# Performance work log

Hardware: AMD Instinct MI355X
Metric: run time of the kernel (lower is better)

The kernel has to match this reference:

```python
import jax, jax.numpy as jnp
import numpy as np
from jax import lax

K = 3          # kernel_size
G = 8          # group count in SIFA
EPS = 1e-5     # BN and GN eps


def _bn(x, g, b, m, v):
    # eval-mode BatchNorm2d over channel dim 1
    scale = (g / jnp.sqrt(v + EPS))[None, :, None, None]
    shift = (b - m * g / jnp.sqrt(v + EPS))[None, :, None, None]
    return x * scale + shift


def setup_inputs() -> dict:
    key = jax.random.key(0)
    ks = jax.random.split(key, 20)
    B, C, H, W, OUP = 8, 64, 128, 128, 128
    CE = C * K * K  # expanded channels = 576
    CG = C // G     # channels per group view = 8
    f32 = jnp.float32
    inp = {
        "x": jax.random.normal(ks[0], (B, C, H, W), f32),
        # depthwise generate conv: groups=C, out=C*K^2 -> OIHW [CE,1,K,K]
        "gen_w": jax.random.normal(ks[1], (CE, 1, K, K), f32) * 0.1,
        "gen_bn_g": jnp.ones((CE,), f32) + 0.1 * jax.random.normal(ks[2], (CE,), f32),
        "gen_bn_b": 0.1 * jax.random.normal(ks[3], (CE,), f32),
        "gen_bn_m": 0.05 * jax.random.normal(ks[4], (CE,), f32),
        "gen_bn_v": jax.random.uniform(ks[5], (CE,), f32, 0.5, 1.5),
        # GroupNorm(num_groups=CG, num_channels=CG) affine params
        "gn_w": jnp.ones((CG,), f32) + 0.1 * jax.random.normal(ks[6], (CG,), f32),
        "gn_b": 0.1 * jax.random.normal(ks[7], (CG,), f32),
        # gating params, shape (1, CG, 1, 1)
        "cweight": 0.1 * jax.random.normal(ks[8], (1, CG, 1, 1), f32),
        "cbias": jnp.ones((1, CG, 1, 1), f32) + 0.1 * jax.random.normal(ks[9], (1, CG, 1, 1), f32),
        "sweight": 0.1 * jax.random.normal(ks[10], (1, CG, 1, 1), f32),
        "sbias": jnp.ones((1, CG, 1, 1), f32) + 0.1 * jax.random.normal(ks[11], (1, CG, 1, 1), f32),
        "weights_add": jnp.asarray(0.5, f32),
        # final Conv: C -> OUP, k=K, s=K, p=0, bias=False + BN + SiLU
        "conv_w": jax.random.normal(ks[12], (OUP, C, K, K), f32) * (1.0 / np.sqrt(C * K * K)),
        "conv_bn_g": jnp.ones((OUP,), f32) + 0.1 * jax.random.normal(ks[13], (OUP,), f32),
        "conv_bn_b": 0.1 * jax.random.normal(ks[14], (OUP,), f32),
        "conv_bn_m": 0.05 * jax.random.normal(ks[15], (OUP,), f32),
        "conv_bn_v": jax.random.uniform(ks[16], (OUP,), f32, 0.5, 1.5),
    }
    return inp


def reference(x, gen_w, gen_bn_g, gen_bn_b, gen_bn_m, gen_bn_v,
              gn_w, gn_b, cweight, cbias, sweight, sbias, weights_add,
              conv_w, conv_bn_g, conv_bn_b, conv_bn_m, conv_bn_v):
    B, C, H, W = x.shape
    # --- generate: depthwise conv (groups=C) + BN + ReLU ---
    y = lax.conv_general_dilated(
        x, gen_w, window_strides=(1, 1), padding=[(K // 2, K // 2)] * 2,
        feature_group_count=C,
        dimension_numbers=("NCHW", "OIHW", "NCHW"))  # [B, C*K*K, H, W]
    y = jax.nn.relu(_bn(y, gen_bn_g, gen_bn_b, gen_bn_m, gen_bn_v))
    # --- rearrange 'b c (n1 n2) h w -> b c (h n1) (w n2)' ---
    y = y.reshape(B, C, K, K, H, W)          # (b, c, n1, n2, h, w)
    y = y.transpose(0, 1, 4, 2, 5, 3)        # (b, c, h, n1, w, n2)
    HK, WK = H * K, W * K
    y = y.reshape(B, C, HK, WK)
    # --- group view: (b*G, C//G, HK, WK) ---
    g = y.reshape(B * G, C // G, HK, WK)
    # channel gate: global avg pool -> affine -> sigmoid
    x_ch = jnp.mean(g, axis=(2, 3), keepdims=True)        # [B*G, CG, 1, 1]
    ch = g * jax.nn.sigmoid(cweight * x_ch + cbias)
    # spatial gate: per-channel GroupNorm (num_groups == num_channels)
    mu = jnp.mean(g, axis=(2, 3), keepdims=True)
    var = jnp.var(g, axis=(2, 3), keepdims=True)
    gnorm = (g - mu) / jnp.sqrt(var + EPS)
    gnorm = gnorm * gn_w[None, :, None, None] + gn_b[None, :, None, None]
    sp = g * jax.nn.sigmoid(sweight * gnorm + sbias)
    out = weights_add * ch + (1.0 - weights_add) * sp
    out = out.reshape(B, C, HK, WK)
    # --- final Conv: k=K, s=K, p=0, no bias + BN + SiLU ---
    z = lax.conv_general_dilated(
        out, conv_w, window_strides=(K, K), padding="VALID",
        dimension_numbers=("NCHW", "OIHW", "NCHW"))       # [B, OUP, H, W]
    z = _bn(z, conv_bn_g, conv_bn_b, conv_bn_m, conv_bn_v)
    return z * jax.nn.sigmoid(z)  # SiLU
```

## Files before the change

### kernel.cpp

```cpp
#include <hip/hip_runtime.h>
#include <math.h>


#define EPSF 1e-5f
typedef _Float16 v8h __attribute__((ext_vector_type(8)));
typedef float v4f __attribute__((ext_vector_type(4)));

static constexpr int C_ = 64, HW_ = 16384, W_ = 128;

static constexpr int WS_WFOLD = 0;
static constexpr int WS_SHIFT = 5184;
static constexpr int WS_BIAS  = 5760;
static constexpr int WS_GATE  = 5888;
static constexpr int WS_PART  = 7936;
static constexpr int WS_WH    = 12032;

__device__ __forceinline__ float sigmf(float v) { return 1.f / (1.f + __expf(-v)); }

__global__ __launch_bounds__(256) void k_fold(
    const float* __restrict__ gen_w,
    const float* __restrict__ gg, const float* __restrict__ gb,
    const float* __restrict__ gm, const float* __restrict__ gv,
    const float* __restrict__ conv_w,
    const float* __restrict__ cg, const float* __restrict__ cb,
    const float* __restrict__ cm, const float* __restrict__ cv,
    float* __restrict__ ws)
{
    int idx = blockIdx.x * 256 + threadIdx.x;
    _Float16* Whp = (_Float16*)(ws + WS_WH);
    if (idx < 131072) {
        int oup = idx >> 10, kk = idx & 1023, c = kk >> 4, j = kk & 15;
        float s = cg[oup] * rsqrtf(cv[oup] + EPSF);
        float v = (j < 9) ? conv_w[(oup * C_ + c) * 9 + j] * s : 0.f;
        Whp[idx] = (_Float16)v;
    } else if (idx < 136256) {
        int i = idx - 131072; int ce = i / 9;
        float s = gg[ce] * rsqrtf(gv[ce] + EPSF);
        ws[WS_WFOLD + i] = gen_w[i] * s;
    } else if (idx < 136832) {
        int ce = idx - 136256;
        float s = gg[ce] * rsqrtf(gv[ce] + EPSF);
        ws[WS_SHIFT + ce] = gb[ce] - gm[ce] * s;
    } else if (idx < 136960) {
        int oup = idx - 136832;
        float s = cg[oup] * rsqrtf(cv[oup] + EPSF);
        ws[WS_BIAS + oup] = cb[oup] - cm[oup] * s;
    }
}

__global__ __launch_bounds__(256) void k_stats(
    const float* __restrict__ x, const float* __restrict__ ws,
    float* __restrict__ part)
{
    __shared__ float xs[34 * 132];
    __shared__ float r1[256], r2[256];
    int bid = blockIdx.x; int b = bid >> 8; int c = (bid >> 2) & 63; int q = bid & 3;
    int t = threadIdx.x;
    const float* xp = x + (size_t)(b * C_ + c) * HW_;
    for (int i = t; i < 4420; i += 256) {
        int r = i / 130, cc = i - r * 130;
        int yy = q * 32 + r - 1, xx = cc - 1;
        float v = 0.f;
        if (yy >= 0 && yy < 128 && xx >= 0 && xx < 128) v = xp[yy * 128 + xx];
        xs[r * 132 + cc] = v;
    }
    __syncthreads();
    const float* wf = ws + WS_WFOLD + c * 81;
    const float* sh = ws + WS_SHIFT + c * 9;
    float s1 = 0.f, s2 = 0.f;
    for (int i = 0; i < 16; ++i) {
        int id = i * 256 + t; int row = id >> 7, col = id & 127;
        float nb[9];
#pragma unroll
        for (int dy = 0; dy < 3; ++dy)
#pragma unroll
            for (int dx = 0; dx < 3; ++dx) nb[dy * 3 + dx] = xs[(row + dy) * 132 + col + dx];
#pragma unroll
        for (int j = 0; j < 9; ++j) {
            float v = sh[j];
#pragma unroll
            for (int k = 0; k < 9; ++k) v = fmaf(wf[j * 9 + k], nb[k], v);
            v = fmaxf(v, 0.f);
            s1 += v; s2 = fmaf(v, v, s2);
        }
    }
    r1[t] = s1; r2[t] = s2;
    __syncthreads();
    for (int s = 128; s > 0; s >>= 1) {
        if (t < s) { r1[t] += r1[t + s]; r2[t] += r2[t + s]; }
        __syncthreads();
    }
    if (t == 0) { part[bid * 2] = r1[0]; part[bid * 2 + 1] = r2[0]; }
}

__global__ __launch_bounds__(256) void k_gate(
    const float* __restrict__ part,
    const float* __restrict__ cwt, const float* __restrict__ cbs,
    const float* __restrict__ swt, const float* __restrict__ sbs,
    const float* __restrict__ gnw, const float* __restrict__ gnb,
    const float* __restrict__ wadd, float4* __restrict__ gate)
{
    int i = blockIdx.x * 256 + threadIdx.x;
    if (i >= 512) return;
    int b = i >> 6, c = i & 63;
    float s1 = 0.f, s2 = 0.f;
    for (int q = 0; q < 4; ++q) {
        int pi = (b * 256 + c * 4 + q) * 2;
        s1 += part[pi]; s2 += part[pi + 1];
    }
    const float N = 9.f * 16384.f;
    float mean = s1 / N;
    float var = s2 / N - mean * mean;
    float inv = rsqrtf(var + EPSF);
    int cgi = c & 7;
    float wa = wadd[0];
    float cgt = sigmf(cwt[cgi] * mean + cbs[cgi]);
    float4 o;
    o.x = wa * cgt;
    o.y = 1.f - wa;
    o.z = swt[cgi] * gnw[cgi] * inv;
    o.w = swt[cgi] * (gnb[cgi] - mean * inv * gnw[cgi]) + sbs[cgi];
    gate[i] = o;
}

__global__ __launch_bounds__(256) void k_main(
    const float* __restrict__ x, const float* __restrict__ ws,
    float* __restrict__ out)
{
    __shared__ _Float16 W_s[128 * 64];
    __shared__ _Float16 u_s[128 * 64];
    __shared__ float xs4[4 * 200];
    __shared__ float bias_s[128];

    int t = threadIdx.x;
    int bid = blockIdx.x;
    int b = bid >> 7, tile = bid & 127;
    int oh0 = (tile >> 3) << 3, ow0 = (tile & 7) << 4;
    if (t < 128) bias_s[t] = ws[WS_BIAS + t];

    const float* xb = x + (size_t)b * C_ * HW_;
    const _Float16* Wh = (const _Float16*)(ws + WS_WH);

    int lane = t & 63, w = t >> 6, quad = lane >> 4, l15 = lane & 15;
    int p = t & 127, cc0 = t >> 7;
    int py = p >> 4, px = p & 15;

    v4f acc[4][4];
#pragma unroll
    for (int a = 0; a < 4; ++a)
#pragma unroll
        for (int bb = 0; bb < 4; ++bb) acc[a][bb] = (v4f)0.f;

    for (int it = 0; it < 16; ++it) {
        int c0 = it * 4;
        __syncthreads();
        for (int i = t; i < 720; i += 256) {
            int ch = i / 180; int rem = i - ch * 180; int r = rem / 18; int cl = rem - r * 18;
            int yy = oh0 + r - 1, xx = ow0 + cl - 1;
            float v = 0.f;
            if (yy >= 0 && yy < 128 && xx >= 0 && xx < 128) v = xb[(c0 + ch) * HW_ + yy * 128 + xx];
            xs4[ch * 200 + r * 20 + cl] = v;
        }
#pragma unroll
        for (int i = 0; i < 4; ++i) {
            int id = t + i * 256; int oup = id >> 3, kb = id & 7;
            float4 v = *(const float4*)(Wh + oup * 1024 + it * 64 + kb * 8);
            *(float4*)&W_s[oup * 64 + ((kb ^ (oup & 7)) << 3)] = v;
        }
        __syncthreads();
#pragma unroll
        for (int uit = 0; uit < 2; ++uit) {
            int cc = cc0 + uit * 2;
            int cs = __builtin_amdgcn_readfirstlane(c0 + cc);
            const float* wfp = ws + WS_WFOLD + cs * 81;
            const float* shp = ws + WS_SHIFT + cs * 9;
            const float* gp  = ws + WS_GATE + (((b << 6) + cs) << 2);
            float gx = gp[0], gy = gp[1], gz = gp[2], gw = gp[3];
            float nb[9];
#pragma unroll
            for (int dy = 0; dy < 3; ++dy)
#pragma unroll
                for (int dx = 0; dx < 3; ++dx)
                    nb[dy * 3 + dx] = xs4[cc * 200 + (py + dy) * 20 + px + dx];
            float uv[9];
#pragma unroll
            for (int j = 0; j < 9; ++j) uv[j] = shp[j];
#pragma unroll
            for (int k = 0; k < 9; ++k) {
                float xv = nb[k];
#pragma unroll
                for (int j = 0; j < 9; ++j) uv[j] = fmaf(wfp[j * 9 + k], xv, uv[j]);
            }
            union { _Float16 h[16]; float4 q[2]; } pk;
#pragma unroll
            for (int j = 0; j < 9; ++j) {
                float v = fmaxf(uv[j], 0.f);
                float g2 = fmaf(gy, sigmf(fmaf(gz, v, gw)), gx);
                pk.h[j] = (_Float16)(v * g2);
            }
#pragma unroll
            for (int j = 9; j < 16; ++j) pk.h[j] = (_Float16)0.f;
            int b0 = cc * 2;
            *(float4*)&u_s[p * 64 + ((b0 ^ (p & 7)) << 3)] = pk.q[0];
            *(float4*)&u_s[p * 64 + (((b0 + 1) ^ (p & 7)) << 3)] = pk.q[1];
        }
        __syncthreads();
#pragma unroll
        for (int ks = 0; ks < 2; ++ks) {
            int kb = ks * 4 + quad;
            v8h A[4], Bf[4];
#pragma unroll
            for (int a = 0; a < 4; ++a) {
                int row = ((w & 1) << 6) + (a << 4) + l15;
                A[a] = *(const v8h*)&W_s[row * 64 + ((kb ^ (row & 7)) << 3)];
            }
#pragma unroll
            for (int bb = 0; bb < 4; ++bb) {
                int row = ((w >> 1) << 6) + (bb << 4) + l15;
                Bf[bb] = *(const v8h*)&u_s[row * 64 + ((kb ^ (row & 7)) << 3)];
            }
#pragma unroll
            for (int a = 0; a < 4; ++a)
#pragma unroll
                for (int bb = 0; bb < 4; ++bb)
                    acc[a][bb] = __builtin_amdgcn_mfma_f32_16x16x32_f16(A[a], Bf[bb], acc[a][bb], 0, 0, 0);
        }
    }

    size_t ob = (size_t)b * 128 * HW_;
#pragma unroll
    for (int a = 0; a < 4; ++a) {
#pragma unroll
        for (int r = 0; r < 4; ++r) {
            int oup = ((w & 1) << 6) + (a << 4) + (quad << 2) + r;
            float bo = bias_s[oup];
#pragma unroll
            for (int bb = 0; bb < 4; ++bb) {
                int p2 = ((w >> 1) << 6) + (bb << 4) + l15;
                int py2 = p2 >> 4, px2 = p2 & 15;
                float z = acc[a][bb][r] + bo;
                out[ob + (size_t)oup * HW_ + (oh0 + py2) * W_ + ow0 + px2] = z * sigmf(z);
            }
        }
    }
}

extern "C" void kernel_launch(void* const* d_in, const int* in_sizes, int n_in,
                              void* d_out, int out_size, void* d_ws, size_t ws_size,
                              hipStream_t stream)
{
    const float* x      = (const float*)d_in[0];
    const float* gen_w  = (const float*)d_in[1];
    const float* gg     = (const float*)d_in[2];
    const float* gb     = (const float*)d_in[3];
    const float* gm     = (const float*)d_in[4];
    const float* gv     = (const float*)d_in[5];
    const float* gnw    = (const float*)d_in[6];
    const float* gnb    = (const float*)d_in[7];
    const float* cwt    = (const float*)d_in[8];
    const float* cbs    = (const float*)d_in[9];
    const float* swt    = (const float*)d_in[10];
    const float* sbs    = (const float*)d_in[11];
    const float* wadd   = (const float*)d_in[12];
    const float* conv_w = (const float*)d_in[13];
    const float* cg2    = (const float*)d_in[14];
    const float* cb2    = (const float*)d_in[15];
    const float* cm2    = (const float*)d_in[16];
    const float* cv2    = (const float*)d_in[17];
    float* ws  = (float*)d_ws;
    float* out = (float*)d_out;

    k_fold<<<535, 256, 0, stream>>>(gen_w, gg, gb, gm, gv, conv_w, cg2, cb2, cm2, cv2, ws);
    k_stats<<<2048, 256, 0, stream>>>(x, ws, ws + WS_PART);
    k_gate<<<2, 256, 0, stream>>>(ws + WS_PART, cwt, cbs, swt, sbs, gnw, gnb, wadd,
                                  (float4*)(ws + WS_GATE));
    k_main<<<1024, 256, 0, stream>>>(x, ws, out);
}
```

Measured before the change: 273.9 us.

## Shrink main-kernel tile, double-buffer input halo, load conv weights directly to registers

The main fused kernel now covers an 8x8 pixel tile per block, so twice as many blocks launch. Each wave owns one channel per iteration and double-buffers that channel's input halo in shared memory, prefetching the next channel while the MFMAs run. The conv weight fragments are read straight from global/L2 into registers instead of being staged through LDS, which drops one LDS buffer and one barrier per iteration. The sigmoid gate uses exp2 and rcp intrinsics with the -log2(e) factor folded into the gate constants, and fp16 packing uses cvt_pkrtz; the stats kernel's inner loop is also reordered. In exchange, each block redoes more halo work relative to its output and issues more global weight reads.

```diff
diff --git a/kernel.cpp b/kernel.cpp
--- a/kernel.cpp
+++ b/kernel.cpp
@@ -4,6 +4,7 @@
 
 #define EPSF 1e-5f
 typedef _Float16 v8h __attribute__((ext_vector_type(8)));
+typedef __fp16 fp16x2 __attribute__((ext_vector_type(2)));
 typedef float v4f __attribute__((ext_vector_type(4)));
 
 static constexpr int C_ = 64, HW_ = 16384, W_ = 128;
@@ -75,12 +76,18 @@
         for (int dy = 0; dy < 3; ++dy)
 #pragma unroll
             for (int dx = 0; dx < 3; ++dx) nb[dy * 3 + dx] = xs[(row + dy) * 132 + col + dx];
+        float uv[9];
+#pragma unroll
+        for (int j = 0; j < 9; ++j) uv[j] = sh[j];
+#pragma unroll
+        for (int k = 0; k < 9; ++k) {
+            float xv = nb[k];
+#pragma unroll
+            for (int j = 0; j < 9; ++j) uv[j] = fmaf(wf[j * 9 + k], xv, uv[j]);
+        }
 #pragma unroll
         for (int j = 0; j < 9; ++j) {
-            float v = sh[j];
-#pragma unroll
-            for (int k = 0; k < 9; ++k) v = fmaf(wf[j * 9 + k], nb[k], v);
-            v = fmaxf(v, 0.f);
+            float v = fmaxf(uv[j], 0.f);
             s1 += v; s2 = fmaf(v, v, s2);
         }
     }
@@ -115,11 +122,12 @@
     int cgi = c & 7;
     float wa = wadd[0];
     float cgt = sigmf(cwt[cgi] * mean + cbs[cgi]);
+    const float NL2E = -1.44269504f;
     float4 o;
     o.x = wa * cgt;
     o.y = 1.f - wa;
-    o.z = swt[cgi] * gnw[cgi] * inv;
-    o.w = swt[cgi] * (gnb[cgi] - mean * inv * gnw[cgi]) + sbs[cgi];
+    o.z = NL2E * (swt[cgi] * gnw[cgi] * inv);
+    o.w = NL2E * (swt[cgi] * (gnb[cgi] - mean * inv * gnw[cgi]) + sbs[cgi]);
     gate[i] = o;
 }
 
@@ -127,104 +135,134 @@
     const float* __restrict__ x, const float* __restrict__ ws,
     float* __restrict__ out)
 {
-    __shared__ _Float16 W_s[128 * 64];
-    __shared__ _Float16 u_s[128 * 64];
-    __shared__ float xs4[4 * 200];
+    __shared__ _Float16 u_s[64 * 64];
+    __shared__ float xs[2][4 * 120];
     __shared__ float bias_s[128];
 
     int t = threadIdx.x;
     int bid = blockIdx.x;
-    int b = bid >> 7, tile = bid & 127;
-    int oh0 = (tile >> 3) << 3, ow0 = (tile & 7) << 4;
+    int b = bid >> 8, tile = bid & 255;
+    int oh0 = (tile >> 4) << 3, ow0 = (tile & 15) << 3;
     if (t < 128) bias_s[t] = ws[WS_BIAS + t];
 
     const float* xb = x + (size_t)b * C_ * HW_;
     const _Float16* Wh = (const _Float16*)(ws + WS_WH);
 
-    int lane = t & 63, w = t >> 6, quad = lane >> 4, l15 = lane & 15;
-    int p = t & 127, cc0 = t >> 7;
-    int py = p >> 4, px = p & 15;
-
-    v4f acc[4][4];
+    int w = __builtin_amdgcn_readfirstlane(t >> 6);
+    int lane = t & 63, quad = lane >> 4, l15 = lane & 15;
+    int py = lane >> 3, px = lane & 7;
+
+    v4f acc[4][2];
 #pragma unroll
     for (int a = 0; a < 4; ++a)
 #pragma unroll
-        for (int bb = 0; bb < 4; ++bb) acc[a][bb] = (v4f)0.f;
-
+        for (int bb = 0; bb < 2; ++bb) acc[a][bb] = (v4f)0.f;
+
+    {
+        const float* xc = xb + (size_t)w * HW_;
+#pragma unroll
+        for (int i = 0; i < 2; ++i) {
+            int item = lane + i * 64;
+            if (item < 100) {
+                int r = item / 10, cl = item - r * 10;
+                int yy = oh0 + r - 1, xx = ow0 + cl - 1;
+                float v = 0.f;
+                if (yy >= 0 && yy < 128 && xx >= 0 && xx < 128) v = xc[yy * 128 + xx];
+                xs[0][w * 120 + r * 12 + cl] = v;
+            }
+        }
+    }
+    __syncthreads();
+
+    int buf = 0;
     for (int it = 0; it < 16; ++it) {
-        int c0 = it * 4;
+        int c = it * 4 + w;
+        const float* wfp = ws + WS_WFOLD + c * 81;
+        const float* shp = ws + WS_SHIFT + c * 9;
+        float4 g4 = *(const float4*)(ws + WS_GATE + (((b << 6) + c) << 2));
+
+        float nb[9];
+        const float* xw = &xs[buf][w * 120];
+#pragma unroll
+        for (int dy = 0; dy < 3; ++dy)
+#pragma unroll
+            for (int dx = 0; dx < 3; ++dx)
+                nb[dy * 3 + dx] = xw[(py + dy) * 12 + px + dx];
+        float uv[9];
+#pragma unroll
+        for (int j = 0; j < 9; ++j) uv[j] = shp[j];
+#pragma unroll
+        for (int k = 0; k < 9; ++k) {
+            float xv = nb[k];
+#pragma unroll
+            for (int j = 0; j < 9; ++j) uv[j] = fmaf(wfp[j * 9 + k], xv, uv[j]);
+        }
+        float ug[9];
+#pragma unroll
+        for (int j = 0; j < 9; ++j) {
+            float v = fmaxf(uv[j], 0.f);
+            float e = __builtin_amdgcn_exp2f(fmaf(g4.z, v, g4.w));
+            float g2 = fmaf(g4.y, __builtin_amdgcn_rcpf(1.f + e), g4.x);
+            ug[j] = v * g2;
+        }
+        union { fp16x2 p[8]; float4 f[2]; } pk;
+        pk.p[0] = __builtin_amdgcn_cvt_pkrtz(ug[0], ug[1]);
+        pk.p[1] = __builtin_amdgcn_cvt_pkrtz(ug[2], ug[3]);
+        pk.p[2] = __builtin_amdgcn_cvt_pkrtz(ug[4], ug[5]);
+        pk.p[3] = __builtin_amdgcn_cvt_pkrtz(ug[6], ug[7]);
+        pk.p[4] = __builtin_amdgcn_cvt_pkrtz(ug[8], 0.f);
+        pk.p[5] = __builtin_amdgcn_cvt_pkrtz(0.f, 0.f);
+        pk.p[6] = __builtin_amdgcn_cvt_pkrtz(0.f, 0.f);
+        pk.p[7] = __builtin_amdgcn_cvt_pkrtz(0.f, 0.f);
+        {
+            int g0 = 2 * w;
+            *(float4*)&u_s[lane * 64 + ((g0 ^ (lane & 7)) << 3)] = pk.f[0];
+            *(float4*)&u_s[lane * 64 + (((g0 + 1) ^ (lane & 7)) << 3)] = pk.f[1];
+        }
+
+        v8h A[2][4];
+#pragma unroll
+        for (int ks = 0; ks < 2; ++ks)
+#pragma unroll
+            for (int a = 0; a < 4; ++a) {
+                int row = ((w & 1) << 6) + (a << 4) + l15;
+                A[ks][a] = *(const v8h*)(Wh + (size_t)row * 1024 + it * 64 + ((ks * 4 + quad) << 3));
+            }
         __syncthreads();
-        for (int i = t; i < 720; i += 256) {
-            int ch = i / 180; int rem = i - ch * 180; int r = rem / 18; int cl = rem - r * 18;
-            int yy = oh0 + r - 1, xx = ow0 + cl - 1;
-            float v = 0.f;
-            if (yy >= 0 && yy < 128 && xx >= 0 && xx < 128) v = xb[(c0 + ch) * HW_ + yy * 128 + xx];
-            xs4[ch * 200 + r * 20 + cl] = v;
-        }
-#pragma unroll
-        for (int i = 0; i < 4; ++i) {
-            int id = t + i * 256; int oup = id >> 3, kb = id & 7;
-            float4 v = *(const float4*)(Wh + oup * 1024 + it * 64 + kb * 8);
-            *(float4*)&W_s[oup * 64 + ((kb ^ (oup & 7)) << 3)] = v;
-        }
-        __syncthreads();
-#pragma unroll
-        for (int uit = 0; uit < 2; ++uit) {
-            int cc = cc0 + uit * 2;
-            int cs = __builtin_amdgcn_readfirstlane(c0 + cc);
-            const float* wfp = ws + WS_WFOLD + cs * 81;
-            const float* shp = ws + WS_SHIFT + cs * 9;
-            const float* gp  = ws + WS_GATE + (((b << 6) + cs) << 2);
-            float gx = gp[0], gy = gp[1], gz = gp[2], gw = gp[3];
-            float nb[9];
-#pragma unroll
-            for (int dy = 0; dy < 3; ++dy)
-#pragma unroll
-                for (int dx = 0; dx < 3; ++dx)
-                    nb[dy * 3 + dx] = xs4[cc * 200 + (py + dy) * 20 + px + dx];
-            float uv[9];
-#pragma unroll
-            for (int j = 0; j < 9; ++j) uv[j] = shp[j];
-#pragma unroll
-            for (int k = 0; k < 9; ++k) {
-                float xv = nb[k];
-#pragma unroll
-                for (int j = 0; j < 9; ++j) uv[j] = fmaf(wfp[j * 9 + k], xv, uv[j]);
-            }
-            union { _Float16 h[16]; float4 q[2]; } pk;
-#pragma unroll
-            for (int j = 0; j < 9; ++j) {
-                float v = fmaxf(uv[j], 0.f);
-                float g2 = fmaf(gy, sigmf(fmaf(gz, v, gw)), gx);
-                pk.h[j] = (_Float16)(v * g2);
-            }
-#pragma unroll
-            for (int j = 9; j < 16; ++j) pk.h[j] = (_Float16)0.f;
-            int b0 = cc * 2;
-            *(float4*)&u_s[p * 64 + ((b0 ^ (p & 7)) << 3)] = pk.q[0];
-            *(float4*)&u_s[p * 64 + (((b0 + 1) ^ (p & 7)) << 3)] = pk.q[1];
-        }
-        __syncthreads();
+
+        if (it < 15) {
+            int cn = (it + 1) * 4 + w;
+            const float* xc = xb + (size_t)cn * HW_;
+#pragma unroll
+            for (int i = 0; i < 2; ++i) {
+                int item = lane + i * 64;
+                if (item < 100) {
+                    int r = item / 10, cl = item - r * 10;
+                    int yy = oh0 + r - 1, xx = ow0 + cl - 1;
+                    float v = 0.f;
+                    if (yy >= 0 && yy < 128 && xx >= 0 && xx < 128) v = xc[yy * 128 + xx];
+                    xs[buf ^ 1][w * 120 + r * 12 + cl] = v;
+                }
+            }
+        }
+
 #pragma unroll
         for (int ks = 0; ks < 2; ++ks) {
             int kb = ks * 4 + quad;
-            v8h A[4], Bf[4];
-#pragma unroll
-            for (int a = 0; a < 4; ++a) {
-                int row = ((w & 1) << 6) + (a << 4) + l15;
-                A[a] = *(const v8h*)&W_s[row * 64 + ((kb ^ (row & 7)) << 3)];
-            }
-#pragma unroll
-            for (int bb = 0; bb < 4; ++bb) {
-                int row = ((w >> 1) << 6) + (bb << 4) + l15;
+            v8h Bf[2];
+#pragma unroll
+            for (int bb = 0; bb < 2; ++bb) {
+                int row = ((w >> 1) << 5) + (bb << 4) + l15;
                 Bf[bb] = *(const v8h*)&u_s[row * 64 + ((kb ^ (row & 7)) << 3)];
             }
 #pragma unroll
             for (int a = 0; a < 4; ++a)
 #pragma unroll
-                for (int bb = 0; bb < 4; ++bb)
-                    acc[a][bb] = __builtin_amdgcn_mfma_f32_16x16x32_f16(A[a], Bf[bb], acc[a][bb], 0, 0, 0);
-        }
+                for (int bb = 0; bb < 2; ++bb)
+                    acc[a][bb] = __builtin_amdgcn_mfma_f32_16x16x32_f16(A[ks][a], Bf[bb], acc[a][bb], 0, 0, 0);
+        }
+        __syncthreads();
+        buf ^= 1;
     }
 
     size_t ob = (size_t)b * 128 * HW_;
@@ -235,9 +273,9 @@
             int oup = ((w & 1) << 6) + (a << 4) + (quad << 2) + r;
             float bo = bias_s[oup];
 #pragma unroll
-            for (int bb = 0; bb < 4; ++bb) {
-                int p2 = ((w >> 1) << 6) + (bb << 4) + l15;
-                int py2 = p2 >> 4, px2 = p2 & 15;
+            for (int bb = 0; bb < 2; ++bb) {
+                int p2 = ((w >> 1) << 5) + (bb << 4) + l15;
+                int py2 = p2 >> 3, px2 = p2 & 7;
                 float z = acc[a][bb][r] + bo;
                 out[ob + (size_t)oup * HW_ + (oh0 + py2) * W_ + ow0 + px2] = z * sigmf(z);
             }
@@ -274,5 +312,5 @@
     k_stats<<<2048, 256, 0, stream>>>(x, ws, ws + WS_PART);
     k_gate<<<2, 256, 0, stream>>>(ws + WS_PART, cwt, cbs, swt, sbs, gnw, gnb, wadd,
                                   (float4*)(ws + WS_GATE));
-    k_main<<<1024, 256, 0, stream>>>(x, ws, out);
-}
+    k_main<<<2048, 256, 0, stream>>>(x, ws, out);
+}
```

Measured after the change: 289.6 us. +5.7%, slower.

## Double-buffer input halo, restructure generate-conv per wave, fold log2e into gate

Applied to the files above, without the earlier changes.

k_main now double-buffers the input halo tile so the next channel group's loads overlap the current MFMA step. The W tile global loads are hoisted into registers early. Each wave computes one channel for two pixel rows, reusing neighbour rows across rows, and the sigmoid uses exp2/rcp intrinsics with -log2e pre-folded into the gate coefficients. k_stats caches the folded weights in LDS and registers instead of reloading them from global memory. The costs are higher register pressure and an extra barrier per iteration.

```diff
diff --git a/kernel.cpp b/kernel.cpp
--- a/kernel.cpp
+++ b/kernel.cpp
@@ -4,6 +4,7 @@
 
 #define EPSF 1e-5f
 typedef _Float16 v8h __attribute__((ext_vector_type(8)));
+typedef __fp16 fp16x2 __attribute__((ext_vector_type(2)));
 typedef float v4f __attribute__((ext_vector_type(4)));
 
 static constexpr int C_ = 64, HW_ = 16384, W_ = 128;
@@ -53,6 +54,8 @@
     float* __restrict__ part)
 {
     __shared__ float xs[34 * 132];
+    __shared__ __align__(16) float wfl[84];
+    __shared__ float shl[9];
     __shared__ float r1[256], r2[256];
     int bid = blockIdx.x; int b = bid >> 8; int c = (bid >> 2) & 63; int q = bid & 3;
     int t = threadIdx.x;
@@ -64,9 +67,17 @@
         if (yy >= 0 && yy < 128 && xx >= 0 && xx < 128) v = xp[yy * 128 + xx];
         xs[r * 132 + cc] = v;
     }
+    if (t < 84) wfl[t] = ws[WS_WFOLD + c * 81 + ((t < 81) ? t : 80)];
+    if (t >= 84 && t < 93) shl[t - 84] = ws[WS_SHIFT + c * 9 + (t - 84)];
     __syncthreads();
-    const float* wf = ws + WS_WFOLD + c * 81;
-    const float* sh = ws + WS_SHIFT + c * 9;
+
+    float wv[84];
+#pragma unroll
+    for (int i = 0; i < 21; ++i) *(float4*)&wv[i * 4] = *(const float4*)&wfl[i * 4];
+    float sh9[9];
+#pragma unroll
+    for (int i = 0; i < 9; ++i) sh9[i] = shl[i];
+
     float s1 = 0.f, s2 = 0.f;
     for (int i = 0; i < 16; ++i) {
         int id = i * 256 + t; int row = id >> 7, col = id & 127;
@@ -75,12 +86,18 @@
         for (int dy = 0; dy < 3; ++dy)
 #pragma unroll
             for (int dx = 0; dx < 3; ++dx) nb[dy * 3 + dx] = xs[(row + dy) * 132 + col + dx];
+        float uv[9];
+#pragma unroll
+        for (int j = 0; j < 9; ++j) uv[j] = sh9[j];
+#pragma unroll
+        for (int k = 0; k < 9; ++k) {
+            float xv = nb[k];
+#pragma unroll
+            for (int j = 0; j < 9; ++j) uv[j] = fmaf(wv[j * 9 + k], xv, uv[j]);
+        }
 #pragma unroll
         for (int j = 0; j < 9; ++j) {
-            float v = sh[j];
-#pragma unroll
-            for (int k = 0; k < 9; ++k) v = fmaf(wf[j * 9 + k], nb[k], v);
-            v = fmaxf(v, 0.f);
+            float v = fmaxf(uv[j], 0.f);
             s1 += v; s2 = fmaf(v, v, s2);
         }
     }
@@ -115,11 +132,12 @@
     int cgi = c & 7;
     float wa = wadd[0];
     float cgt = sigmf(cwt[cgi] * mean + cbs[cgi]);
+    const float NL2E = -1.44269504f;
     float4 o;
     o.x = wa * cgt;
     o.y = 1.f - wa;
-    o.z = swt[cgi] * gnw[cgi] * inv;
-    o.w = swt[cgi] * (gnb[cgi] - mean * inv * gnw[cgi]) + sbs[cgi];
+    o.z = NL2E * (swt[cgi] * gnw[cgi] * inv);
+    o.w = NL2E * (swt[cgi] * (gnb[cgi] - mean * inv * gnw[cgi]) + sbs[cgi]);
     gate[i] = o;
 }
 
@@ -127,23 +145,24 @@
     const float* __restrict__ x, const float* __restrict__ ws,
     float* __restrict__ out)
 {
+    __shared__ _Float16 u_s[128 * 64];
     __shared__ _Float16 W_s[128 * 64];
-    __shared__ _Float16 u_s[128 * 64];
-    __shared__ float xs4[4 * 200];
+    __shared__ float xs[2][4 * 200];
     __shared__ float bias_s[128];
 
     int t = threadIdx.x;
     int bid = blockIdx.x;
     int b = bid >> 7, tile = bid & 127;
-    int oh0 = (tile >> 3) << 3, ow0 = (tile & 7) << 4;
+    int oh0 = (tile >> 3) << 3;
+    int ow0 = (tile & 7) << 4;
     if (t < 128) bias_s[t] = ws[WS_BIAS + t];
 
     const float* xb = x + (size_t)b * C_ * HW_;
     const _Float16* Wh = (const _Float16*)(ws + WS_WH);
 
-    int lane = t & 63, w = t >> 6, quad = lane >> 4, l15 = lane & 15;
-    int p = t & 127, cc0 = t >> 7;
-    int py = p >> 4, px = p & 15;
+    int w = __builtin_amdgcn_readfirstlane(t >> 6);
+    int lane = t & 63, quad = lane >> 4, l15 = lane & 15;
+    int col = lane & 15, prow0 = (lane >> 4) << 1;
 
     v4f acc[4][4];
 #pragma unroll
@@ -151,60 +170,119 @@
 #pragma unroll
         for (int bb = 0; bb < 4; ++bb) acc[a][bb] = (v4f)0.f;
 
+    {
+        const float* xc = xb + (size_t)w * HW_;
+#pragma unroll
+        for (int i = 0; i < 3; ++i) {
+            int item = lane + i * 64;
+            if (item < 180) {
+                int r = item / 18, cl = item - r * 18;
+                int yy = oh0 + r - 1, xx = ow0 + cl - 1;
+                float v = 0.f;
+                if (yy >= 0 && yy < 128 && xx >= 0 && xx < 128) v = xc[yy * 128 + xx];
+                xs[0][w * 200 + r * 20 + cl] = v;
+            }
+        }
+    }
+    __syncthreads();
+
+    int buf = 0;
     for (int it = 0; it < 16; ++it) {
-        int c0 = it * 4;
-        __syncthreads();
-        for (int i = t; i < 720; i += 256) {
-            int ch = i / 180; int rem = i - ch * 180; int r = rem / 18; int cl = rem - r * 18;
-            int yy = oh0 + r - 1, xx = ow0 + cl - 1;
-            float v = 0.f;
-            if (yy >= 0 && yy < 128 && xx >= 0 && xx < 128) v = xb[(c0 + ch) * HW_ + yy * 128 + xx];
-            xs4[ch * 200 + r * 20 + cl] = v;
-        }
+        int c = it * 4 + w;
+
+        float4 wld[4];
 #pragma unroll
         for (int i = 0; i < 4; ++i) {
             int id = t + i * 256; int oup = id >> 3, kb = id & 7;
-            float4 v = *(const float4*)(Wh + oup * 1024 + it * 64 + kb * 8);
-            *(float4*)&W_s[oup * 64 + ((kb ^ (oup & 7)) << 3)] = v;
+            wld[i] = *(const float4*)(Wh + oup * 1024 + it * 64 + kb * 8);
+        }
+
+        const float* xw = &xs[buf][w * 200];
+        float nb[12];
+#pragma unroll
+        for (int dr = 0; dr < 4; ++dr)
+#pragma unroll
+            for (int dc = 0; dc < 3; ++dc)
+                nb[dr * 3 + dc] = xw[(prow0 + dr) * 20 + col + dc];
+
+        const float* wfp = ws + WS_WFOLD + c * 81;
+        const float* shp = ws + WS_SHIFT + c * 9;
+        float4 g4 = *(const float4*)(ws + WS_GATE + (((b << 6) + c) << 2));
+
+        int p0 = prow0 * 16 + col;
+        int swzA0 = ((2 * w) ^ (p0 & 7)) << 3;
+        int swzA1 = ((2 * w) ^ ((p0 + 16) & 7)) << 3;
+        int swzB0 = ((2 * w + 1) ^ (p0 & 7)) << 3;
+        int swzB1 = ((2 * w + 1) ^ ((p0 + 16) & 7)) << 3;
+
+#pragma unroll 1
+        for (int jp = 0; jp < 4; ++jp) {
+            float wl[18];
+#pragma unroll
+            for (int i = 0; i < 18; ++i) wl[i] = wfp[jp * 18 + i];
+            float s0 = shp[jp * 2], s1v = shp[jp * 2 + 1];
+#pragma unroll
+            for (int px = 0; px < 2; ++px) {
+                float a0 = s0, a1 = s1v;
+#pragma unroll
+                for (int k = 0; k < 9; ++k) {
+                    float xv = nb[(px + k / 3) * 3 + (k % 3)];
+                    a0 = fmaf(wl[k], xv, a0);
+                    a1 = fmaf(wl[9 + k], xv, a1);
+                }
+                float v0 = fmaxf(a0, 0.f), v1 = fmaxf(a1, 0.f);
+                float e0 = __builtin_amdgcn_exp2f(fmaf(g4.z, v0, g4.w));
+                float e1 = __builtin_amdgcn_exp2f(fmaf(g4.z, v1, g4.w));
+                float u0 = v0 * fmaf(g4.y, __builtin_amdgcn_rcpf(1.f + e0), g4.x);
+                float u1 = v1 * fmaf(g4.y, __builtin_amdgcn_rcpf(1.f + e1), g4.x);
+                int base = (p0 + px * 16) * 64 + (px ? swzA1 : swzA0);
+                *(fp16x2*)&u_s[base + jp * 2] = __builtin_amdgcn_cvt_pkrtz(u0, u1);
+            }
+        }
+        {
+            float w9[9];
+#pragma unroll
+            for (int i = 0; i < 9; ++i) w9[i] = wfp[72 + i];
+            float s8 = shp[8];
+#pragma unroll
+            for (int px = 0; px < 2; ++px) {
+                float a0 = s8;
+#pragma unroll
+                for (int k = 0; k < 9; ++k)
+                    a0 = fmaf(w9[k], nb[(px + k / 3) * 3 + (k % 3)], a0);
+                float v0 = fmaxf(a0, 0.f);
+                float e0 = __builtin_amdgcn_exp2f(fmaf(g4.z, v0, g4.w));
+                float u8 = v0 * fmaf(g4.y, __builtin_amdgcn_rcpf(1.f + e0), g4.x);
+                union { fp16x2 p[4]; float4 f; } z;
+                z.p[0] = __builtin_amdgcn_cvt_pkrtz(u8, 0.f);
+                z.p[1] = __builtin_amdgcn_cvt_pkrtz(0.f, 0.f);
+                z.p[2] = z.p[1]; z.p[3] = z.p[1];
+                int base = (p0 + px * 16) * 64 + (px ? swzB1 : swzB0);
+                *(float4*)&u_s[base] = z.f;
+            }
+        }
+
+#pragma unroll
+        for (int i = 0; i < 4; ++i) {
+            int id = t + i * 256; int oup = id >> 3, kb = id & 7;
+            *(float4*)&W_s[oup * 64 + ((kb ^ (oup & 7)) << 3)] = wld[i];
+        }
+        if (it < 15) {
+            const float* xc = xb + (size_t)(it * 4 + 4 + w) * HW_;
+#pragma unroll
+            for (int i = 0; i < 3; ++i) {
+                int item = lane + i * 64;
+                if (item < 180) {
+                    int r = item / 18, cl = item - r * 18;
+                    int yy = oh0 + r - 1, xx = ow0 + cl - 1;
+                    float v = 0.f;
+                    if (yy >= 0 && yy < 128 && xx >= 0 && xx < 128) v = xc[yy * 128 + xx];
+                    xs[buf ^ 1][w * 200 + r * 20 + cl] = v;
+                }
+            }
         }
         __syncthreads();
-#pragma unroll
-        for (int uit = 0; uit < 2; ++uit) {
-            int cc = cc0 + uit * 2;
-            int cs = __builtin_amdgcn_readfirstlane(c0 + cc);
-            const float* wfp = ws + WS_WFOLD + cs * 81;
-            const float* shp = ws + WS_SHIFT + cs * 9;
-            const float* gp  = ws + WS_GATE + (((b << 6) + cs) << 2);
-            float gx = gp[0], gy = gp[1], gz = gp[2], gw = gp[3];
-            float nb[9];
-#pragma unroll
-            for (int dy = 0; dy < 3; ++dy)
-#pragma unroll
-                for (int dx = 0; dx < 3; ++dx)
-                    nb[dy * 3 + dx] = xs4[cc * 200 + (py + dy) * 20 + px + dx];
-            float uv[9];
-#pragma unroll
-            for (int j = 0; j < 9; ++j) uv[j] = shp[j];
-#pragma unroll
-            for (int k = 0; k < 9; ++k) {
-                float xv = nb[k];
-#pragma unroll
-                for (int j = 0; j < 9; ++j) uv[j] = fmaf(wfp[j * 9 + k], xv, uv[j]);
-            }
-            union { _Float16 h[16]; float4 q[2]; } pk;
-#pragma unroll
-            for (int j = 0; j < 9; ++j) {
-                float v = fmaxf(uv[j], 0.f);
-                float g2 = fmaf(gy, sigmf(fmaf(gz, v, gw)), gx);
-                pk.h[j] = (_Float16)(v * g2);
-            }
-#pragma unroll
-            for (int j = 9; j < 16; ++j) pk.h[j] = (_Float16)0.f;
-            int b0 = cc * 2;
-            *(float4*)&u_s[p * 64 + ((b0 ^ (p & 7)) << 3)] = pk.q[0];
-            *(float4*)&u_s[p * 64 + (((b0 + 1) ^ (p & 7)) << 3)] = pk.q[1];
-        }
-        __syncthreads();
+
 #pragma unroll
         for (int ks = 0; ks < 2; ++ks) {
             int kb = ks * 4 + quad;
@@ -225,6 +303,8 @@
                 for (int bb = 0; bb < 4; ++bb)
                     acc[a][bb] = __builtin_amdgcn_mfma_f32_16x16x32_f16(A[a], Bf[bb], acc[a][bb], 0, 0, 0);
         }
+        __syncthreads();
+        buf ^= 1;
     }
 
     size_t ob = (size_t)b * 128 * HW_;
```

Result: faster. 252.6 us (-7.8%).
